# Optimization experiments

Hardware: AMD Instinct MI355X
Metric: run time of the kernel (lower is better)

## Reference

```python
import jax, jax.numpy as jnp
import numpy as np

B, T, D, H = 2, 2048, 1024, 16
DH = D // H


def setup_inputs() -> dict:
    key = jax.random.key(0)
    ks = jax.random.split(key, 5)
    scale = 1.0 / np.sqrt(D)
    return {
        "x": jax.random.normal(ks[0], (B, T, D), dtype=jnp.float32),
        "Wq": jax.random.normal(ks[1], (D, D), dtype=jnp.float32) * scale,
        "Wk": jax.random.normal(ks[2], (D, D), dtype=jnp.float32) * scale,
        "Wv": jax.random.normal(ks[3], (D, D), dtype=jnp.float32) * scale,
        "Wo": jax.random.normal(ks[4], (D, D), dtype=jnp.float32) * scale,
    }


def _split(y):
    # (B,T,D) -> (B,H,T,DH)
    b, t, _ = y.shape
    return y.reshape(b, t, H, DH).transpose(0, 2, 1, 3)


def reference(x, Wq, Wk, Wv, Wo):
    q = _split(x @ Wq)
    k = _split(x @ Wk)
    v = _split(x @ Wv)
    scores = jnp.einsum("bhqd,bhkd->bhqk", q, k) / jnp.sqrt(jnp.float32(DH))
    t = x.shape[1]
    # additive causal mask: -1e9 above the diagonal (matches band_part logic)
    causal = jnp.tril(jnp.ones((t, t), dtype=jnp.float32))
    scores = scores + (1.0 - causal) * -1e9
    attn = jax.nn.softmax(scores, axis=-1)
    out = jnp.einsum("bhqk,bhkd->bhqd", attn, v)  # (B,H,T,DH)
    out = out.transpose(0, 2, 1, 3).reshape(x.shape[0], t, D)
    return out @ Wo
```

## Files before the change

kernel.cpp:

```cpp
#include <hip/hip_runtime.h>

#define BB 2
#define TT 2048
#define DD 1024
#define HH 16
#define DHD 64
#define MM (BB*TT)

typedef __attribute__((ext_vector_type(8))) short short8;
typedef __attribute__((ext_vector_type(4))) float float4v;
typedef unsigned short u16;

__device__ inline float bf2f(u16 u) {
    union { unsigned int i; float f; } v;
    v.i = ((unsigned int)u) << 16;
    return v.f;
}
__device__ inline u16 f2bf(float f) {
    union { float f; unsigned int i; } v;
    v.f = f;
    unsigned int x = v.i;
    unsigned int r = (x + 0x7fffu + ((x >> 16) & 1u)) >> 16;
    return (u16)r;
}

__global__ __launch_bounds__(256) void cast_x_k(const float* __restrict__ x,
                                                u16* __restrict__ xb) {
    int i = blockIdx.x * 256 + threadIdx.x;
    float4v v = ((const float4v*)x)[i];
    ushort4 o;
    o.x = f2bf(v[0]); o.y = f2bf(v[1]); o.z = f2bf(v[2]); o.w = f2bf(v[3]);
    ((ushort4*)xb)[i] = o;
}

__global__ __launch_bounds__(256) void transw_k(const float* __restrict__ Wq,
                                                const float* __restrict__ Wk,
                                                const float* __restrict__ Wv,
                                                const float* __restrict__ Wo,
                                                u16* __restrict__ WT) {
    __shared__ u16 t[32][33];
    int wsel = blockIdx.z;
    const float* W = (wsel == 0) ? Wq : (wsel == 1) ? Wk : (wsel == 2) ? Wv : Wo;
    u16* o = WT + (size_t)wsel * DD * DD;
    int k0 = blockIdx.y * 32, n0 = blockIdx.x * 32;
    int tx = threadIdx.x, ty = threadIdx.y;
#pragma unroll
    for (int i = 0; i < 4; i++) {
        int k = ty + i * 8;
        t[k][tx] = f2bf(W[(size_t)(k0 + k) * DD + n0 + tx]);
    }
    __syncthreads();
#pragma unroll
    for (int i = 0; i < 4; i++) {
        int n = ty + i * 8;
        o[(size_t)(n0 + n) * DD + k0 + tx] = t[tx][n];
    }
}

template <int MODE, int TM, int TN>
__global__ __launch_bounds__(256) void gemm_k(const u16* __restrict__ A,
                                              const u16* __restrict__ WT0,
                                              void* __restrict__ outp) {
    const int K = DD, BK = 64;
    const int MT = TM / 32, NT = TN / 32;
    const int NS = (TM + TN) * (BK / 8) / 256;

    int z = blockIdx.z;
    const u16* WT = WT0 + (size_t)z * DD * DD;
    int n0 = blockIdx.x * TN, m0 = blockIdx.y * TM;

    __shared__ u16 S[(TM + TN) * BK];

    int tid = threadIdx.x;
    int lane = tid & 63, w = tid >> 6;
    int wm = (w >> 1) * (TM / 2), wn = (w & 1) * (TN / 2);
    int quad = lane >> 4, l16 = lane & 15;

    const u16* gp[NS];
    u16* lp[NS];
#pragma unroll
    for (int j = 0; j < NS; j++) {
        int cid = tid + j * 256;
        int r = cid >> 3, c = cid & 7;
        lp[j] = S + r * BK + (c ^ (r & 7)) * 8;
        gp[j] = (r < TM ? A + (size_t)(m0 + r) * K
                        : WT + (size_t)(n0 + r - TM) * K) + c * 8;
    }
    int swz = l16 & 7;

    float4v acc[MT][NT];
#pragma unroll
    for (int i = 0; i < MT; i++)
#pragma unroll
        for (int j = 0; j < NT; j++) acc[i][j] = (float4v)(0.0f);

    short8 pr[NS];
#pragma unroll
    for (int j = 0; j < NS; j++) pr[j] = *(const short8*)gp[j];

    const int NK = K / BK;
#pragma unroll 1
    for (int ki = 0; ki < NK; ki++) {
        __syncthreads();
#pragma unroll
        for (int j = 0; j < NS; j++) *(short8*)lp[j] = pr[j];
        __syncthreads();

        if (ki + 1 < NK) {
            int k0 = (ki + 1) * BK;
#pragma unroll
            for (int j = 0; j < NS; j++) pr[j] = *(const short8*)(gp[j] + k0);
        }

#pragma unroll
        for (int ks = 0; ks < 2; ks++) {
            int cq = ((ks * 4 + quad) ^ swz) * 8;
            short8 a[MT], b[NT];
#pragma unroll
            for (int mt = 0; mt < MT; mt++)
                a[mt] = *(const short8*)&S[(wm + mt * 16 + l16) * BK + cq];
#pragma unroll
            for (int nt = 0; nt < NT; nt++)
                b[nt] = *(const short8*)&S[(TM + wn + nt * 16 + l16) * BK + cq];
#pragma unroll
            for (int mt = 0; mt < MT; mt++)
#pragma unroll
                for (int nt = 0; nt < NT; nt++)
                    acc[mt][nt] = __builtin_amdgcn_mfma_f32_16x16x32_bf16(
                        a[mt], b[nt], acc[mt][nt], 0, 0, 0);
        }
    }

#pragma unroll
    for (int mt = 0; mt < MT; mt++) {
#pragma unroll
        for (int nt = 0; nt < NT; nt++) {
#pragma unroll
            for (int r = 0; r < 4; r++) {
                int m = m0 + wm + mt * 16 + quad * 4 + r;
                int n = n0 + wn + nt * 16 + l16;
                float v = acc[mt][nt][r];
                if constexpr (MODE == 0) {
                    int bb = m >> 11, t = m & 2047;
                    int h = n >> 6, dh = n & 63;
                    size_t idx;
                    if (z == 2)
                        idx = (((size_t)2 * BB * HH + bb * HH + h) * DHD + dh) * TT + t;
                    else
                        idx = (((size_t)z * BB * HH + bb * HH + h) * TT + t) * DHD + dh;
                    ((u16*)outp)[idx] = f2bf(v);
                } else {
                    ((float*)outp)[(size_t)m * DD + n] = v;
                }
            }
        }
    }
}

__global__ __launch_bounds__(256) void attn_k(const u16* __restrict__ QKV,
                                              u16* __restrict__ AO) {
    const u16* Q  = QKV;
    const u16* Kp = QKV + (size_t)MM * DD;
    const u16* Vp = QKV + (size_t)2 * MM * DD;
    int bh = blockIdx.y;
    int p  = blockIdx.x;
    int qA = p, qB = 31 - p;
    size_t hoff = (size_t)bh * TT * DHD;

    __shared__ u16 Qs[2][64][72];
    __shared__ u16 Ks[2][64][72];
    __shared__ u16 VTs[2][64][72];
    __shared__ u16 Ps[4][16][72];

    int tid = threadIdx.x;
    int lane = tid & 63, w = tid >> 6;
    int quad = lane >> 4, l16 = lane & 15;

    int srow[4], scc[4];
#pragma unroll
    for (int i = 0; i < 4; i++) {
        int c = tid + i * 256;
        srow[i] = c >> 4;
        scc[i]  = (c & 15) * 4;
    }

    const float qscale = 0.125f * 1.4426950408889634f;
#pragma unroll
    for (int t = 0; t < 2; t++) {
        int q0 = (t ? qB : qA) * 64;
#pragma unroll
        for (int i = 0; i < 4; i++) {
            ushort4 v = *(const ushort4*)(Q + hoff + (size_t)(q0 + srow[i]) * DHD + scc[i]);
            ushort4 sv;
            sv.x = f2bf(bf2f(v.x) * qscale);
            sv.y = f2bf(bf2f(v.y) * qscale);
            sv.z = f2bf(bf2f(v.z) * qscale);
            sv.w = f2bf(bf2f(v.w) * qscale);
            *(ushort4*)&Qs[t][srow[i]][scc[i]] = sv;
        }
    }

    ushort4 kreg[4], vreg[4];
#pragma unroll
    for (int i = 0; i < 4; i++) {
        kreg[i] = *(const ushort4*)(Kp + hoff + (size_t)srow[i] * DHD + scc[i]);
        vreg[i] = *(const ushort4*)(Vp + hoff + (size_t)srow[i] * TT + scc[i]);
    }

    __syncthreads();
    short8 aqA0 = *(const short8*)&Qs[0][w * 16 + l16][quad * 8];
    short8 aqA1 = *(const short8*)&Qs[0][w * 16 + l16][32 + quad * 8];
    short8 aqB0 = *(const short8*)&Qs[1][w * 16 + l16][quad * 8];
    short8 aqB1 = *(const short8*)&Qs[1][w * 16 + l16][32 + quad * 8];

    int b = bh >> 4, h = bh & 15;
    int it = 0;

#pragma unroll 1
    for (int phase = 0; phase < 2; phase++) {
        int qt = phase ? qB : qA;
        int ntile = qt + 1;
        short8 aq0 = phase ? aqB0 : aqA0;
        short8 aq1 = phase ? aqB1 : aqA1;

        float4v o[4];
#pragma unroll
        for (int i = 0; i < 4; i++) o[i] = (float4v)(0.0f);
        float lr = 0.0f;

#pragma unroll 1
        for (int jt = 0; jt < ntile; jt++, it++) {
            int db = it & 1;
#pragma unroll
            for (int i = 0; i < 4; i++) {
                *(ushort4*)&Ks[db][srow[i]][scc[i]]  = kreg[i];
                *(ushort4*)&VTs[db][srow[i]][scc[i]] = vreg[i];
            }
            __syncthreads();

            bool last = (phase == 1) && (jt == ntile - 1);
            if (!last) {
                int nj = (jt + 1 < ntile) ? (jt + 1) * 64 : 0;
#pragma unroll
                for (int i = 0; i < 4; i++) {
                    kreg[i] = *(const ushort4*)(Kp + hoff + (size_t)(nj + srow[i]) * DHD + scc[i]);
                    vreg[i] = *(const ushort4*)(Vp + hoff + (size_t)srow[i] * TT + nj + scc[i]);
                }
            }

            float4v s[4];
#pragma unroll
            for (int ct = 0; ct < 4; ct++) {
                short8 ak0 = *(const short8*)&Ks[db][ct * 16 + l16][quad * 8];
                short8 ak1 = *(const short8*)&Ks[db][ct * 16 + l16][32 + quad * 8];
                float4v sv = (float4v)(0.0f);
                sv = __builtin_amdgcn_mfma_f32_16x16x32_bf16(ak0, aq0, sv, 0, 0, 0);
                sv = __builtin_amdgcn_mfma_f32_16x16x32_bf16(ak1, aq1, sv, 0, 0, 0);
                s[ct] = sv;
            }

            if (jt == ntile - 1) {
                int ql = w * 16 + l16;
#pragma unroll
                for (int ct = 0; ct < 4; ct++)
#pragma unroll
                    for (int r = 0; r < 4; r++) {
                        int kvl = ct * 16 + quad * 4 + r;
                        if (kvl > ql) s[ct][r] = -30000.0f;
                    }
            }

#pragma unroll
            for (int ct = 0; ct < 4; ct++) {
                float p0 = exp2f(s[ct][0]);
                float p1 = exp2f(s[ct][1]);
                float p2 = exp2f(s[ct][2]);
                float p3 = exp2f(s[ct][3]);
                lr += (p0 + p1) + (p2 + p3);
                union { float f; unsigned u; } c0, c1, c2, c3;
                c0.f = p0; c1.f = p1; c2.f = p2; c3.f = p3;
                ushort4 pw;
                pw.x = (u16)(c0.u >> 16);
                pw.y = (u16)(c1.u >> 16);
                pw.z = (u16)(c2.u >> 16);
                pw.w = (u16)(c3.u >> 16);
                *(ushort4*)&Ps[w][l16][ct * 16 + quad * 4] = pw;
            }

            short8 ap0 = *(const short8*)&Ps[w][l16][quad * 8];
            short8 ap1 = *(const short8*)&Ps[w][l16][32 + quad * 8];
#pragma unroll
            for (int ct = 0; ct < 4; ct++) {
                short8 bv0 = *(const short8*)&VTs[db][ct * 16 + l16][quad * 8];
                short8 bv1 = *(const short8*)&VTs[db][ct * 16 + l16][32 + quad * 8];
                o[ct] = __builtin_amdgcn_mfma_f32_16x16x32_bf16(ap0, bv0, o[ct], 0, 0, 0);
                o[ct] = __builtin_amdgcn_mfma_f32_16x16x32_bf16(ap1, bv1, o[ct], 0, 0, 0);
            }
        }

        float rs = lr;
        rs += __shfl_xor(rs, 16);
        rs += __shfl_xor(rs, 32);
        int gbase = lane & 48;
        float rinv[4];
#pragma unroll
        for (int r = 0; r < 4; r++)
            rinv[r] = 1.0f / __shfl(rs, gbase + quad * 4 + r);

        int q0 = qt * 64;
#pragma unroll
        for (int ct = 0; ct < 4; ct++) {
#pragma unroll
            for (int r = 0; r < 4; r++) {
                int q = q0 + w * 16 + quad * 4 + r;
                int d = h * 64 + ct * 16 + l16;
                AO[(size_t)(b * TT + q) * DD + d] = f2bf(o[ct][r] * rinv[r]);
            }
        }
    }
}

extern "C" void kernel_launch(void* const* d_in, const int* in_sizes, int n_in,
                              void* d_out, int out_size, void* d_ws, size_t ws_size,
                              hipStream_t stream) {
    const float* x  = (const float*)d_in[0];
    const float* Wq = (const float*)d_in[1];
    const float* Wk = (const float*)d_in[2];
    const float* Wv = (const float*)d_in[3];
    const float* Wo = (const float*)d_in[4];

    u16* xb  = (u16*)d_ws;
    u16* WT  = xb + (size_t)MM * DD;
    u16* QKV = WT + (size_t)4 * DD * DD;
    u16* AO  = QKV + (size_t)3 * MM * DD;
    float* out = (float*)d_out;

    cast_x_k<<<dim3(MM * DD / 1024), 256, 0, stream>>>(x, xb);
    transw_k<<<dim3(32, 32, 4), dim3(32, 8), 0, stream>>>(Wq, Wk, Wv, Wo, WT);
    gemm_k<0, 128, 128><<<dim3(DD / 128, MM / 128, 3), 256, 0, stream>>>(xb, WT, QKV);
    attn_k<<<dim3(16, 32), 256, 0, stream>>>(QKV, AO);
    gemm_k<1, 64, 128><<<dim3(DD / 128, MM / 64, 1), 256, 0, stream>>>(AO, WT + (size_t)3 * DD * DD, out);
}
```

Measured before the change: 188.5 us.

## Process both paired query tiles concurrently with 512-thread attention blocks and swizzled LDS

The attention kernel now runs 8 waves per block. Two groups of 4 waves each own one of the paired query tiles (p and 31-p) and share a single pass over K/V tiles, where before the two tiles were processed one after the other. Shared-memory tiles drop the padding and use an XOR swizzle with 16-byte loads and stores to avoid bank conflicts. A tile-index swizzle spreads work across blocks. This halves the serial K/V sweep per block and removes padding, at the cost of idle waves in the shorter group once its tile finishes, and higher per-block register and LDS pressure.

```diff
diff --git a/kernel.cpp b/kernel.cpp
--- a/kernel.cpp
+++ b/kernel.cpp
@@ -157,110 +157,89 @@
     }
 }
 
-__global__ __launch_bounds__(256) void attn_k(const u16* __restrict__ QKV,
+__global__ __launch_bounds__(512) void attn_k(const u16* __restrict__ QKV,
                                               u16* __restrict__ AO) {
     const u16* Q  = QKV;
     const u16* Kp = QKV + (size_t)MM * DD;
     const u16* Vp = QKV + (size_t)2 * MM * DD;
     int bh = blockIdx.y;
-    int p  = blockIdx.x;
+    int tswz = (blockIdx.x + blockIdx.y) & 15;
+    int p = (blockIdx.y & 16) ? (15 - tswz) : tswz;
     int qA = p, qB = 31 - p;
     size_t hoff = (size_t)bh * TT * DHD;
 
-    __shared__ u16 Qs[2][64][72];
-    __shared__ u16 Ks[2][64][72];
-    __shared__ u16 VTs[2][64][72];
-    __shared__ u16 Ps[4][16][72];
+    __shared__ u16 Qs[2][64 * 64];
+    __shared__ u16 Ks[2][64 * 64];
+    __shared__ u16 VTs[2][64 * 64];
+    __shared__ u16 Ps[8][16 * 64];
 
     int tid = threadIdx.x;
-    int lane = tid & 63, w = tid >> 6;
+    int lane = tid & 63, wv = tid >> 6;
+    int g = wv >> 2, w4 = wv & 3;
     int quad = lane >> 4, l16 = lane & 15;
 
-    int srow[4], scc[4];
-#pragma unroll
-    for (int i = 0; i < 4; i++) {
-        int c = tid + i * 256;
-        srow[i] = c >> 4;
-        scc[i]  = (c & 15) * 4;
-    }
+    int sr = tid >> 3, sc = tid & 7;
+    int sl = sr * 64 + ((sc ^ (sr & 7)) * 8);
+    const u16* gK = Kp + hoff + (size_t)sr * DHD + sc * 8;
+    const u16* gV = Vp + hoff + (size_t)sr * TT + sc * 8;
 
     const float qscale = 0.125f * 1.4426950408889634f;
 #pragma unroll
     for (int t = 0; t < 2; t++) {
         int q0 = (t ? qB : qA) * 64;
-#pragma unroll
-        for (int i = 0; i < 4; i++) {
-            ushort4 v = *(const ushort4*)(Q + hoff + (size_t)(q0 + srow[i]) * DHD + scc[i]);
-            ushort4 sv;
-            sv.x = f2bf(bf2f(v.x) * qscale);
-            sv.y = f2bf(bf2f(v.y) * qscale);
-            sv.z = f2bf(bf2f(v.z) * qscale);
-            sv.w = f2bf(bf2f(v.w) * qscale);
-            *(ushort4*)&Qs[t][srow[i]][scc[i]] = sv;
-        }
-    }
-
-    ushort4 kreg[4], vreg[4];
-#pragma unroll
-    for (int i = 0; i < 4; i++) {
-        kreg[i] = *(const ushort4*)(Kp + hoff + (size_t)srow[i] * DHD + scc[i]);
-        vreg[i] = *(const ushort4*)(Vp + hoff + (size_t)srow[i] * TT + scc[i]);
-    }
+        short8 v = *(const short8*)(Q + hoff + (size_t)(q0 + sr) * DHD + sc * 8);
+        short8 sv;
+#pragma unroll
+        for (int e = 0; e < 8; e++) sv[e] = (short)f2bf(bf2f((u16)v[e]) * qscale);
+        *(short8*)&Qs[t][sl] = sv;
+    }
+
+    short8 prK = *(const short8*)gK;
+    short8 prV = *(const short8*)gV;
 
     __syncthreads();
-    short8 aqA0 = *(const short8*)&Qs[0][w * 16 + l16][quad * 8];
-    short8 aqA1 = *(const short8*)&Qs[0][w * 16 + l16][32 + quad * 8];
-    short8 aqB0 = *(const short8*)&Qs[1][w * 16 + l16][quad * 8];
-    short8 aqB1 = *(const short8*)&Qs[1][w * 16 + l16][32 + quad * 8];
-
-    int b = bh >> 4, h = bh & 15;
-    int it = 0;
+    int cxs = l16 & 7;
+    int fr = w4 * 16 + l16;
+    short8 aq0 = *(const short8*)&Qs[g][fr * 64 + ((quad ^ cxs) * 8)];
+    short8 aq1 = *(const short8*)&Qs[g][fr * 64 + (((4 + quad) ^ cxs) * 8)];
+
+    int myqt = g ? qB : qA;
+    int ntile = myqt + 1;
+    int NR = qB + 1;
+
+    float4v o[4];
+#pragma unroll
+    for (int i = 0; i < 4; i++) o[i] = (float4v)(0.0f);
+    float lr = 0.0f;
 
 #pragma unroll 1
-    for (int phase = 0; phase < 2; phase++) {
-        int qt = phase ? qB : qA;
-        int ntile = qt + 1;
-        short8 aq0 = phase ? aqB0 : aqA0;
-        short8 aq1 = phase ? aqB1 : aqA1;
-
-        float4v o[4];
-#pragma unroll
-        for (int i = 0; i < 4; i++) o[i] = (float4v)(0.0f);
-        float lr = 0.0f;
-
-#pragma unroll 1
-        for (int jt = 0; jt < ntile; jt++, it++) {
-            int db = it & 1;
-#pragma unroll
-            for (int i = 0; i < 4; i++) {
-                *(ushort4*)&Ks[db][srow[i]][scc[i]]  = kreg[i];
-                *(ushort4*)&VTs[db][srow[i]][scc[i]] = vreg[i];
-            }
-            __syncthreads();
-
-            bool last = (phase == 1) && (jt == ntile - 1);
-            if (!last) {
-                int nj = (jt + 1 < ntile) ? (jt + 1) * 64 : 0;
-#pragma unroll
-                for (int i = 0; i < 4; i++) {
-                    kreg[i] = *(const ushort4*)(Kp + hoff + (size_t)(nj + srow[i]) * DHD + scc[i]);
-                    vreg[i] = *(const ushort4*)(Vp + hoff + (size_t)srow[i] * TT + nj + scc[i]);
-                }
-            }
-
+    for (int jt = 0; jt < NR; jt++) {
+        int db = jt & 1;
+        *(short8*)&Ks[db][sl]  = prK;
+        *(short8*)&VTs[db][sl] = prV;
+        __syncthreads();
+
+        if (jt + 1 < NR) {
+            size_t nj = (size_t)(jt + 1) * 64;
+            prK = *(const short8*)(gK + nj * DHD);
+            prV = *(const short8*)(gV + nj);
+        }
+
+        if (jt < ntile) {
             float4v s[4];
 #pragma unroll
             for (int ct = 0; ct < 4; ct++) {
-                short8 ak0 = *(const short8*)&Ks[db][ct * 16 + l16][quad * 8];
-                short8 ak1 = *(const short8*)&Ks[db][ct * 16 + l16][32 + quad * 8];
+                int kr = (ct * 16 + l16) * 64;
+                short8 ak0 = *(const short8*)&Ks[db][kr + ((quad ^ cxs) * 8)];
+                short8 ak1 = *(const short8*)&Ks[db][kr + (((4 + quad) ^ cxs) * 8)];
                 float4v sv = (float4v)(0.0f);
                 sv = __builtin_amdgcn_mfma_f32_16x16x32_bf16(ak0, aq0, sv, 0, 0, 0);
                 sv = __builtin_amdgcn_mfma_f32_16x16x32_bf16(ak1, aq1, sv, 0, 0, 0);
                 s[ct] = sv;
             }
 
-            if (jt == ntile - 1) {
-                int ql = w * 16 + l16;
+            if (jt == myqt) {
+                int ql = w4 * 16 + l16;
 #pragma unroll
                 for (int ct = 0; ct < 4; ct++)
 #pragma unroll
@@ -284,38 +263,41 @@
                 pw.y = (u16)(c1.u >> 16);
                 pw.z = (u16)(c2.u >> 16);
                 pw.w = (u16)(c3.u >> 16);
-                *(ushort4*)&Ps[w][l16][ct * 16 + quad * 4] = pw;
-            }
-
-            short8 ap0 = *(const short8*)&Ps[w][l16][quad * 8];
-            short8 ap1 = *(const short8*)&Ps[w][l16][32 + quad * 8];
+                int chnk = (ct * 2 + (quad >> 1)) ^ cxs;
+                *(ushort4*)&Ps[wv][l16 * 64 + chnk * 8 + (quad & 1) * 4] = pw;
+            }
+
+            short8 ap0 = *(const short8*)&Ps[wv][l16 * 64 + ((quad ^ cxs) * 8)];
+            short8 ap1 = *(const short8*)&Ps[wv][l16 * 64 + (((4 + quad) ^ cxs) * 8)];
 #pragma unroll
             for (int ct = 0; ct < 4; ct++) {
-                short8 bv0 = *(const short8*)&VTs[db][ct * 16 + l16][quad * 8];
-                short8 bv1 = *(const short8*)&VTs[db][ct * 16 + l16][32 + quad * 8];
+                int vr = (ct * 16 + l16) * 64;
+                short8 bv0 = *(const short8*)&VTs[db][vr + ((quad ^ cxs) * 8)];
+                short8 bv1 = *(const short8*)&VTs[db][vr + (((4 + quad) ^ cxs) * 8)];
                 o[ct] = __builtin_amdgcn_mfma_f32_16x16x32_bf16(ap0, bv0, o[ct], 0, 0, 0);
                 o[ct] = __builtin_amdgcn_mfma_f32_16x16x32_bf16(ap1, bv1, o[ct], 0, 0, 0);
             }
         }
-
-        float rs = lr;
-        rs += __shfl_xor(rs, 16);
-        rs += __shfl_xor(rs, 32);
-        int gbase = lane & 48;
-        float rinv[4];
-#pragma unroll
-        for (int r = 0; r < 4; r++)
-            rinv[r] = 1.0f / __shfl(rs, gbase + quad * 4 + r);
-
-        int q0 = qt * 64;
-#pragma unroll
-        for (int ct = 0; ct < 4; ct++) {
-#pragma unroll
-            for (int r = 0; r < 4; r++) {
-                int q = q0 + w * 16 + quad * 4 + r;
-                int d = h * 64 + ct * 16 + l16;
-                AO[(size_t)(b * TT + q) * DD + d] = f2bf(o[ct][r] * rinv[r]);
-            }
+    }
+
+    float rs = lr;
+    rs += __shfl_xor(rs, 16);
+    rs += __shfl_xor(rs, 32);
+    int gbase = lane & 48;
+    float rinv[4];
+#pragma unroll
+    for (int r = 0; r < 4; r++)
+        rinv[r] = 1.0f / __shfl(rs, gbase + quad * 4 + r);
+
+    int b = bh >> 4, h = bh & 15;
+    int q0 = myqt * 64;
+#pragma unroll
+    for (int ct = 0; ct < 4; ct++) {
+#pragma unroll
+        for (int r = 0; r < 4; r++) {
+            int q = q0 + w4 * 16 + quad * 4 + r;
+            int d = h * 64 + ct * 16 + l16;
+            AO[(size_t)(b * TT + q) * DD + d] = f2bf(o[ct][r] * rinv[r]);
         }
     }
 }
@@ -338,6 +320,6 @@
     cast_x_k<<<dim3(MM * DD / 1024), 256, 0, stream>>>(x, xb);
     transw_k<<<dim3(32, 32, 4), dim3(32, 8), 0, stream>>>(Wq, Wk, Wv, Wo, WT);
     gemm_k<0, 128, 128><<<dim3(DD / 128, MM / 128, 3), 256, 0, stream>>>(xb, WT, QKV);
-    attn_k<<<dim3(16, 32), 256, 0, stream>>>(QKV, AO);
+    attn_k<<<dim3(16, 32), 512, 0, stream>>>(QKV, AO);
     gemm_k<1, 64, 128><<<dim3(DD / 128, MM / 64, 1), 256, 0, stream>>>(AO, WT + (size_t)3 * DD * DD, out);
 }
```

New measurement: 174.7 us. -7.3%, faster.
